# Optimization experiments

Hardware: AMD Instinct MI355X
Metric: run time of the kernel (lower is better)

## Reference

```python
import jax, jax.numpy as jnp
import numpy as np

EPS_LN = 1e-5
EPS_D = 1e-8
K = 3

def layer_norm(x, g, b):
    mu = jnp.mean(x, axis=-1, keepdims=True)
    var = jnp.var(x, axis=-1, keepdims=True)
    return (x - mu) * jax.lax.rsqrt(var + EPS_LN) * g + b

def setup_inputs() -> dict:
    key = jax.random.key(0)
    ks = jax.random.split(key, 8)
    Nc, Nu, Cin, Cout = 4096, 16384, 256, 256
    return {
        "x_feat": jax.random.normal(ks[0], (Nc, Cin), jnp.float32),
        "x_pos": jax.random.uniform(ks[1], (Nc, 3), jnp.float32),
        "xup_feat": jax.random.normal(ks[2], (Nu, Cout), jnp.float32),
        "xup_pos": jax.random.uniform(ks[3], (Nu, 3), jnp.float32),
        "g1": jnp.ones((Cin,), jnp.float32),
        "b1": jnp.zeros((Cin,), jnp.float32),
        "W": jax.random.normal(ks[4], (Cin, Cout), jnp.float32) * 0.02,
        "b": jnp.zeros((Cout,), jnp.float32),
        "g2": jnp.ones((Cout,), jnp.float32),
        "b2": jnp.zeros((Cout,), jnp.float32),
        "W_up": jax.random.normal(ks[5], (Cout, Cout), jnp.float32) * 0.02,
        "b_up": jnp.zeros((Cout,), jnp.float32),
    }

def reference(x_feat, x_pos, xup_feat, xup_pos, g1, b1, W, b, g2, b2, W_up, b_up):
    # norm -> linear on coarse points: [Nc, Cout]
    x = layer_norm(x_feat, g1, b1) @ W + b
    # norm -> linear on fine points:   [Nu, Cout]
    xu = layer_norm(xup_feat, g2, b2) @ W_up + b_up
    # squared pairwise distances fine->coarse: [Nu, Nc]
    d2 = (jnp.sum(xup_pos * xup_pos, axis=-1, keepdims=True)
          - 2.0 * (xup_pos @ x_pos.T)
          + jnp.sum(x_pos * x_pos, axis=-1))
    # k nearest coarse neighbors per fine point
    neg_d2, idx = jax.lax.top_k(-d2, K)          # [Nu, K]
    w = 1.0 / (-neg_d2 + EPS_D)                  # inverse-distance weights
    w = w / jnp.sum(w, axis=-1, keepdims=True)
    # gather + weighted sum: [Nu, Cout]
    interp = jnp.einsum('uk,ukc->uc', w, x[idx])
    return interp + xu
```

## Files before the change

kernel.cpp:

```cpp
#include <hip/hip_runtime.h>

#define EPS_LN 1e-5f
#define EPS_D  1e-8f
#define BIGD 3.402823466e+38f

typedef __attribute__((ext_vector_type(8))) short s16x8;
typedef __attribute__((ext_vector_type(4))) float f32x4;
typedef __attribute__((ext_vector_type(4))) unsigned short u16x4;

#define XC_OFF    0u
#define XH_OFF    4194304u
#define XL_OFF    14680064u
#define MU_OFF    25165824u
#define RS_OFF    25247744u
#define WGH_OFF   25329664u
#define WGL_OFF   25460736u
#define WUGH_OFF  25591808u
#define WUGL_OFF  25722880u
#define C12_OFF   25853952u
#define CPS_OFF   25858048u
#define IDXS_OFF  25923584u
#define CST_OFF   25939968u
#define UPS_OFF   25944064u
#define USORT_OFF 26206208u

__device__ __forceinline__ int cell_of(float px, float py, float pz) {
    int cx = (int)(px * 8.0f); cx = cx < 0 ? 0 : (cx > 7 ? 7 : cx);
    int cy = (int)(py * 8.0f); cy = cy < 0 ? 0 : (cy > 7 ? 7 : cy);
    int cz = (int)(pz * 8.0f); cz = cz < 0 ? 0 : (cz > 7 ? 7 : cz);
    return (cz * 8 + cy) * 8 + cx;
}

__global__ __launch_bounds__(256) void prep_kernel(
    const float* __restrict__ x_feat, const float* __restrict__ xup_feat,
    const float* __restrict__ x_pos, const float* __restrict__ xup_pos,
    const float* __restrict__ W, const float* __restrict__ W_up,
    const float* __restrict__ g1, const float* __restrict__ b1,
    const float* __restrict__ g2, const float* __restrict__ b2,
    float* __restrict__ mu, float* __restrict__ rs,
    unsigned short* __restrict__ xh, unsigned short* __restrict__ xl,
    unsigned short* __restrict__ wgh, unsigned short* __restrict__ wgl,
    unsigned short* __restrict__ wugh, unsigned short* __restrict__ wugl,
    float* __restrict__ c12,
    float4* __restrict__ cps, int* __restrict__ idxs, int* __restrict__ cellStart,
    float4* __restrict__ ups, int* __restrict__ usort)
{
    __shared__ int cnt[512];
    __shared__ int ofs[512];
    __shared__ int wpart[4];

    const int bid = blockIdx.x, tid = threadIdx.x;
    const int lane = tid & 63, wave = tid >> 6;

    if (bid < 640) {
        #pragma unroll
        for (int rr = 0; rr < 8; ++rr) {
            const int r = bid * 32 + wave * 8 + rr;
            const float* src = (r < 16384) ? (xup_feat + (size_t)r * 256)
                                           : (x_feat + (size_t)(r - 16384) * 256);
            const float4 v = ((const float4*)src)[lane];
            float s  = v.x + v.y + v.z + v.w;
            float ss = v.x*v.x + v.y*v.y + v.z*v.z + v.w*v.w;
            #pragma unroll
            for (int off = 1; off < 64; off <<= 1) {
                s  += __shfl_xor(s,  off);
                ss += __shfl_xor(ss, off);
            }
            if (lane == 0) {
                const float m   = s * (1.0f / 256.0f);
                const float var = ss * (1.0f / 256.0f) - m * m;
                mu[r] = m;
                rs[r] = rsqrtf(var + EPS_LN);
            }
            const float vv[4] = { v.x, v.y, v.z, v.w };
            u16x4 hv, lv;
            #pragma unroll
            for (int c = 0; c < 4; ++c) {
                const unsigned ua = __float_as_uint(vv[c]);
                hv[c] = (unsigned short)(ua >> 16);
                const float lo = vv[c] - __uint_as_float(ua & 0xFFFF0000u);
                lv[c] = (unsigned short)(__float_as_uint(lo) >> 16);
            }
            *(u16x4*)&xh[(size_t)r * 256 + lane * 4] = hv;
            *(u16x4*)&xl[(size_t)r * 256 + lane * 4] = lv;
        }
    } else if (bid < 656) {
        const int mb = bid - 640;
        const float* src = (mb < 8) ? W : W_up;
        const float* g   = (mb < 8) ? g1 : g2;
        unsigned short* dh = (mb < 8) ? wgh : wugh;
        unsigned short* dl = (mb < 8) ? wgl : wugl;
        const int n  = (mb & 7) * 32 + (tid >> 3);
        const int kc = (tid & 7) * 32;
        for (int kk = 0; kk < 32; kk += 4) {
            u16x4 hv, lv;
            #pragma unroll
            for (int c = 0; c < 4; ++c) {
                const int k = kc + kk + c;
                const float wv = g[k] * src[(size_t)k * 256 + n];
                const unsigned ua = __float_as_uint(wv);
                hv[c] = (unsigned short)(ua >> 16);
                const float lo = wv - __uint_as_float(ua & 0xFFFF0000u);
                lv[c] = (unsigned short)(__float_as_uint(lo) >> 16);
            }
            *(u16x4*)&dh[(size_t)n * 256 + kc + kk] = hv;
            *(u16x4*)&dl[(size_t)n * 256 + kc + kk] = lv;
        }
    } else if (bid < 658) {
        const bool fine = (bid == 657);
        const float* src = fine ? W_up : W;
        const float* g   = fine ? g2 : g1;
        const float* bln = fine ? b2 : b1;
        float* c1 = c12 + (fine ? 0 : 512);
        float* c2 = c12 + (fine ? 256 : 768);
        float a1 = 0.0f, a2 = 0.0f;
        for (int k = 0; k < 256; ++k) {
            const float wv = src[(size_t)k * 256 + tid];
            a1 = fmaf(bln[k], wv, a1);
            a2 = fmaf(g[k],   wv, a2);
        }
        c1[tid] = a1;
        c2[tid] = a2;
    } else {
        const bool fine = (bid == 659);
        const int npts = fine ? 16384 : 4096;
        const float* pos = fine ? xup_pos : x_pos;

        cnt[tid] = 0; cnt[tid + 256] = 0;
        __syncthreads();
        for (int i = tid; i < npts; i += 256) {
            const int c = cell_of(pos[i*3+0], pos[i*3+1], pos[i*3+2]);
            atomicAdd(&cnt[c], 1);
        }
        __syncthreads();
        const int base = wave * 128 + lane * 2;
        const int a = cnt[base], b = cnt[base + 1];
        const int p = a + b;
        int incl = p;
        #pragma unroll
        for (int off = 1; off < 64; off <<= 1) {
            const int t = __shfl_up(incl, off);
            if (lane >= off) incl += t;
        }
        if (lane == 63) wpart[wave] = incl;
        __syncthreads();
        int woff = 0;
        for (int w = 0; w < 4; ++w) if (w < wave) woff += wpart[w];
        const int e0 = woff + (incl - p);
        ofs[base] = e0;          ofs[base + 1] = e0 + a;
        if (!fine) {
            cellStart[base] = e0;    cellStart[base + 1] = e0 + a;
            if (tid == 0) cellStart[512] = 4096;
        }
        __syncthreads();
        for (int i = tid; i < npts; i += 256) {
            const float px = pos[i*3+0], py = pos[i*3+1], pz = pos[i*3+2];
            const int c = cell_of(px, py, pz);
            const int slot = atomicAdd(&ofs[c], 1);
            if (fine) {
                ups[slot] = make_float4(px, py, pz, px*px + py*py + pz*pz);
                usort[slot] = i;
            } else {
                cps[slot] = make_float4(px, py, pz, px*px + py*py + pz*pz);
                idxs[slot] = i;
            }
        }
    }
}

__global__ __launch_bounds__(256) void gemm_kernel(
    const unsigned short* __restrict__ xh, const unsigned short* __restrict__ xl,
    const float* __restrict__ mu, const float* __restrict__ rs,
    const unsigned short* __restrict__ wgh, const unsigned short* __restrict__ wgl,
    const unsigned short* __restrict__ wugh, const unsigned short* __restrict__ wugl,
    const float* __restrict__ c12,
    const float* __restrict__ b_up, const float* __restrict__ bb,
    float* __restrict__ outF, float* __restrict__ outC)
{
    const int bid = blockIdx.x;
    const unsigned short *BH, *BL; const float *c1, *c2, *bias; float* OUT;
    int row0, col0, statbase;
    if (bid < 256) {
        BH = wugh; BL = wugl; c1 = c12; c2 = c12 + 256; bias = b_up; OUT = outF;
        row0 = (bid >> 1) * 128; col0 = (bid & 1) * 128; statbase = 0;
    } else {
        const int id = bid - 256;
        BH = wgh; BL = wgl; c1 = c12 + 512; c2 = c12 + 768; bias = bb; OUT = outC;
        row0 = (id >> 1) * 128; col0 = (id & 1) * 128; statbase = 16384;
    }

    const int lane = threadIdx.x & 63;
    const int wave = threadIdx.x >> 6;
    const int wr = wave >> 1, wc = wave & 1;
    const int lm = lane & 15, lk = lane >> 4;

    int arow[4];
    #pragma unroll
    for (int mf = 0; mf < 4; ++mf)
        arow[mf] = statbase + row0 + wr * 64 + mf * 16 + lm;

    int ncol[4]; float c1v[4], c2v[4], bv[4];
    #pragma unroll
    for (int nf = 0; nf < 4; ++nf) {
        ncol[nf] = col0 + wc * 64 + nf * 16 + lm;
        c1v[nf] = c1[ncol[nf]];
        c2v[nf] = c2[ncol[nf]];
        bv[nf]  = bias[ncol[nf]];
    }

    f32x4 acc[4][4];
    #pragma unroll
    for (int mf = 0; mf < 4; ++mf)
        #pragma unroll
        for (int nf = 0; nf < 4; ++nf)
            acc[mf][nf] = (f32x4){0.0f, 0.0f, 0.0f, 0.0f};

    for (int k0 = 0; k0 < 256; k0 += 32) {
        const int kb = k0 + lk * 8;

        s16x8 bh[4], bl[4], ah[4], al[4];
        #pragma unroll
        for (int nf = 0; nf < 4; ++nf) {
            const size_t o = (size_t)ncol[nf] * 256 + kb;
            bh[nf] = *(const s16x8*)(BH + o);
            bl[nf] = *(const s16x8*)(BL + o);
        }
        #pragma unroll
        for (int mf = 0; mf < 4; ++mf) {
            const size_t o = (size_t)arow[mf] * 256 + kb;
            ah[mf] = *(const s16x8*)(xh + o);
            al[mf] = *(const s16x8*)(xl + o);
        }

        #pragma unroll
        for (int mf = 0; mf < 4; ++mf)
            #pragma unroll
            for (int nf = 0; nf < 4; ++nf) {
                acc[mf][nf] = __builtin_amdgcn_mfma_f32_16x16x32_bf16(ah[mf], bh[nf], acc[mf][nf], 0, 0, 0);
                acc[mf][nf] = __builtin_amdgcn_mfma_f32_16x16x32_bf16(ah[mf], bl[nf], acc[mf][nf], 0, 0, 0);
                acc[mf][nf] = __builtin_amdgcn_mfma_f32_16x16x32_bf16(al[mf], bh[nf], acc[mf][nf], 0, 0, 0);
            }
    }

    #pragma unroll
    for (int mf = 0; mf < 4; ++mf) {
        #pragma unroll
        for (int q = 0; q < 4; ++q) {
            const int orow = row0 + wr * 64 + mf * 16 + lk * 4 + q;
            const float m = mu[statbase + orow];
            const float s = rs[statbase + orow];
            const float ms = -m * s;
            #pragma unroll
            for (int nf = 0; nf < 4; ++nf)
                OUT[(size_t)orow * 256 + ncol[nf]] =
                    fmaf(s, acc[mf][nf][q], fmaf(ms, c2v[nf], c1v[nf]) + bv[nf]);
        }
    }
}

__device__ __forceinline__ void ins3(float d, int p,
    float& b0, float& b1, float& b2, int& p0, int& p1, int& p2)
{
    const bool lt0 = d < b0, lt1 = d < b1, lt2 = d < b2;
    const float n1 = lt0 ? b0 : (lt1 ? d : b1);
    const int   q1 = lt0 ? p0 : (lt1 ? p : p1);
    const float n2 = lt1 ? b1 : (lt2 ? d : b2);
    const int   q2 = lt1 ? p1 : (lt2 ? p : p2);
    b0 = lt0 ? d : b0;  p0 = lt0 ? p : p0;
    b1 = n1; p1 = q1;
    b2 = n2; p2 = q2;
}

__global__ __launch_bounds__(256) void topk_kernel(
    const float4* __restrict__ cps, const int* __restrict__ idxs,
    const int* __restrict__ cellStart,
    const float4* __restrict__ ups, const int* __restrict__ usort,
    const float* __restrict__ xc, float* __restrict__ out)
{
    __shared__ float pd[4][64][3];
    __shared__ int   pp[4][64][3];
    __shared__ float wsel[64][3];
    __shared__ int   isel[64][3];
    __shared__ int   uor[64];
    __shared__ int   cst[513];

    const int tid = threadIdx.x, lane = tid & 63, wave = tid >> 6;
    const int su = blockIdx.x * 64 + lane;

    for (int i = tid; i < 513; i += 256) cst[i] = cellStart[i];

    const float4 up = ups[su];
    const float ux = up.x, uy = up.y, uz = up.z, uu = up.w;
    if (wave == 0) uor[lane] = usort[su];
    int cx = (int)(ux * 8.0f); cx = cx < 0 ? 0 : (cx > 7 ? 7 : cx);
    int cy = (int)(uy * 8.0f); cy = cy < 0 ? 0 : (cy > 7 ? 7 : cy);
    int cz = (int)(uz * 8.0f); cz = cz < 0 ? 0 : (cz > 7 ? 7 : cz);

    __syncthreads();

    float b0 = BIGD, b1 = BIGD, b2 = BIGD;
    int p0 = 0, p1 = 0, p2 = 0;

    for (int cc = wave; cc < 27; cc += 4) {
        const int nx = cx + (cc % 3) - 1;
        const int ny = cy + ((cc / 3) % 3) - 1;
        const int nz = cz + (cc / 9) - 1;
        if ((unsigned)nx > 7u || (unsigned)ny > 7u || (unsigned)nz > 7u) continue;
        const int cell = (nz * 8 + ny) * 8 + nx;
        const int s = cst[cell], e = cst[cell + 1];
        if (s >= e) continue;
        float4 c = cps[s];
        for (int p = s; p < e; ++p) {
            const float4 nxt = (p + 1 < e) ? cps[p + 1] : c;
            const float dot = ux * c.x + uy * c.y + uz * c.z;
            const float d = (uu - 2.0f * dot) + c.w;
            ins3(d, p, b0, b1, b2, p0, p1, p2);
            c = nxt;
        }
    }

    pd[wave][lane][0] = b0; pd[wave][lane][1] = b1; pd[wave][lane][2] = b2;
    pp[wave][lane][0] = p0; pp[wave][lane][1] = p1; pp[wave][lane][2] = p2;
    __syncthreads();

    if (wave == 0) {
        for (int w = 1; w < 4; ++w) {
            #pragma unroll
            for (int e = 0; e < 3; ++e)
                ins3(pd[w][lane][e], pp[w][lane][e], b0, b1, b2, p0, p1, p2);
        }

        const float h = 0.125f;
        float gmin = BIGD;
        if (cx > 0) gmin = fminf(gmin, ux - (float)(cx - 1) * h);
        if (cx < 7) gmin = fminf(gmin, (float)(cx + 2) * h - ux);
        if (cy > 0) gmin = fminf(gmin, uy - (float)(cy - 1) * h);
        if (cy < 7) gmin = fminf(gmin, (float)(cy + 2) * h - uy);
        if (cz > 0) gmin = fminf(gmin, uz - (float)(cz - 1) * h);
        if (cz < 7) gmin = fminf(gmin, (float)(cz + 2) * h - uz);

        if (b2 > gmin * gmin) {
            b0 = b1 = b2 = BIGD; p0 = p1 = p2 = 0;
            for (int p = 0; p < 4096; ++p) {
                const float4 c = cps[p];
                const float dot = ux * c.x + uy * c.y + uz * c.z;
                const float d = (uu - 2.0f * dot) + c.w;
                ins3(d, p, b0, b1, b2, p0, p1, p2);
            }
        }

        float w0 = 1.0f / (b0 + EPS_D);
        float w1 = 1.0f / (b1 + EPS_D);
        float w2 = 1.0f / (b2 + EPS_D);
        const float inv = 1.0f / (w0 + w1 + w2);
        wsel[lane][0] = w0 * inv; wsel[lane][1] = w1 * inv; wsel[lane][2] = w2 * inv;
        isel[lane][0] = idxs[p0]; isel[lane][1] = idxs[p1]; isel[lane][2] = idxs[p2];
    }
    __syncthreads();

    #pragma unroll
    for (int r = 0; r < 16; ++r) {
        const int ul = wave * 16 + r;
        const float w0 = wsel[ul][0], w1 = wsel[ul][1], w2 = wsel[ul][2];
        const int a0 = isel[ul][0], a1 = isel[ul][1], a2 = isel[ul][2];
        const float4 v0 = ((const float4*)(xc + (size_t)a0 * 256))[lane];
        const float4 v1 = ((const float4*)(xc + (size_t)a1 * 256))[lane];
        const float4 v2 = ((const float4*)(xc + (size_t)a2 * 256))[lane];
        float4* op = (float4*)(out + (size_t)uor[ul] * 256);
        float4 o = op[lane];
        o.x += w0 * v0.x + w1 * v1.x + w2 * v2.x;
        o.y += w0 * v0.y + w1 * v1.y + w2 * v2.y;
        o.z += w0 * v0.z + w1 * v1.z + w2 * v2.z;
        o.w += w0 * v0.w + w1 * v1.w + w2 * v2.w;
        op[lane] = o;
    }
}

extern "C" void kernel_launch(void* const* d_in, const int* in_sizes, int n_in,
                              void* d_out, int out_size, void* d_ws, size_t ws_size,
                              hipStream_t stream)
{
    const float* x_feat   = (const float*)d_in[0];
    const float* x_pos    = (const float*)d_in[1];
    const float* xup_feat = (const float*)d_in[2];
    const float* xup_pos  = (const float*)d_in[3];
    const float* g1       = (const float*)d_in[4];
    const float* b1       = (const float*)d_in[5];
    const float* W        = (const float*)d_in[6];
    const float* bb       = (const float*)d_in[7];
    const float* g2       = (const float*)d_in[8];
    const float* b2       = (const float*)d_in[9];
    const float* W_up     = (const float*)d_in[10];
    const float* b_up     = (const float*)d_in[11];

    float* out = (float*)d_out;
    char*  ws  = (char*)d_ws;

    float* xc  = (float*)(ws + XC_OFF);
    unsigned short* xh   = (unsigned short*)(ws + XH_OFF);
    unsigned short* xl   = (unsigned short*)(ws + XL_OFF);
    float* mu  = (float*)(ws + MU_OFF);
    float* rs  = (float*)(ws + RS_OFF);
    unsigned short* wgh  = (unsigned short*)(ws + WGH_OFF);
    unsigned short* wgl  = (unsigned short*)(ws + WGL_OFF);
    unsigned short* wugh = (unsigned short*)(ws + WUGH_OFF);
    unsigned short* wugl = (unsigned short*)(ws + WUGL_OFF);
    float* c12 = (float*)(ws + C12_OFF);
    float4* cps = (float4*)(ws + CPS_OFF);
    int* idxs   = (int*)(ws + IDXS_OFF);
    int* cstart = (int*)(ws + CST_OFF);
    float4* ups = (float4*)(ws + UPS_OFF);
    int* usort  = (int*)(ws + USORT_OFF);

    prep_kernel<<<660, 256, 0, stream>>>(x_feat, xup_feat, x_pos, xup_pos,
                                         W, W_up, g1, b1, g2, b2,
                                         mu, rs, xh, xl,
                                         wgh, wgl, wugh, wugl,
                                         c12, cps, idxs, cstart, ups, usort);
    gemm_kernel<<<320, 256, 0, stream>>>(xh, xl, mu, rs,
                                         wgh, wgl, wugh, wugl,
                                         c12, b_up, bb, out, xc);
    topk_kernel<<<256, 256, 0, stream>>>(cps, idxs, cstart, ups, usort, xc, out);
}
```

Measured before the change: 192.4 us.

## Use 1024-thread prep blocks and schedule serial binning blocks first

The prep kernel now runs 168 blocks of 1024 threads instead of 660 blocks of 256. The long serial tasks (spatial binning of points and the c1/c2 bias reductions) move to the lowest block indices so they start first. The c1/c2 reduction is split four ways over k and summed in shared memory, and the scan covers 512 cells with 8 waves. This is meant to shorten the critical path of the binning and reduction blocks that previously trailed the row-wise layer-norm split work. In exchange, fewer and larger blocks may limit how many blocks fit per CU.

```diff
diff --git a/kernel.cpp b/kernel.cpp
--- a/kernel.cpp
+++ b/kernel.cpp
@@ -31,7 +31,7 @@
     return (cz * 8 + cy) * 8 + cx;
 }
 
-__global__ __launch_bounds__(256) void prep_kernel(
+__global__ __launch_bounds__(1024) void prep_kernel(
     const float* __restrict__ x_feat, const float* __restrict__ xup_feat,
     const float* __restrict__ x_pos, const float* __restrict__ xup_pos,
     const float* __restrict__ W, const float* __restrict__ W_up,
@@ -45,115 +45,55 @@
     float4* __restrict__ cps, int* __restrict__ idxs, int* __restrict__ cellStart,
     float4* __restrict__ ups, int* __restrict__ usort)
 {
-    __shared__ int cnt[512];
-    __shared__ int ofs[512];
-    __shared__ int wpart[4];
+    __shared__ float smemf[2048];
+    int* const cnt   = (int*)smemf;
+    int* const ofs   = ((int*)smemf) + 512;
+    __shared__ int wpart[8];
+    __shared__ int wpref[8];
 
     const int bid = blockIdx.x, tid = threadIdx.x;
     const int lane = tid & 63, wave = tid >> 6;
 
-    if (bid < 640) {
-        #pragma unroll
-        for (int rr = 0; rr < 8; ++rr) {
-            const int r = bid * 32 + wave * 8 + rr;
-            const float* src = (r < 16384) ? (xup_feat + (size_t)r * 256)
-                                           : (x_feat + (size_t)(r - 16384) * 256);
-            const float4 v = ((const float4*)src)[lane];
-            float s  = v.x + v.y + v.z + v.w;
-            float ss = v.x*v.x + v.y*v.y + v.z*v.z + v.w*v.w;
-            #pragma unroll
-            for (int off = 1; off < 64; off <<= 1) {
-                s  += __shfl_xor(s,  off);
-                ss += __shfl_xor(ss, off);
-            }
-            if (lane == 0) {
-                const float m   = s * (1.0f / 256.0f);
-                const float var = ss * (1.0f / 256.0f) - m * m;
-                mu[r] = m;
-                rs[r] = rsqrtf(var + EPS_LN);
-            }
-            const float vv[4] = { v.x, v.y, v.z, v.w };
-            u16x4 hv, lv;
-            #pragma unroll
-            for (int c = 0; c < 4; ++c) {
-                const unsigned ua = __float_as_uint(vv[c]);
-                hv[c] = (unsigned short)(ua >> 16);
-                const float lo = vv[c] - __uint_as_float(ua & 0xFFFF0000u);
-                lv[c] = (unsigned short)(__float_as_uint(lo) >> 16);
-            }
-            *(u16x4*)&xh[(size_t)r * 256 + lane * 4] = hv;
-            *(u16x4*)&xl[(size_t)r * 256 + lane * 4] = lv;
-        }
-    } else if (bid < 656) {
-        const int mb = bid - 640;
-        const float* src = (mb < 8) ? W : W_up;
-        const float* g   = (mb < 8) ? g1 : g2;
-        unsigned short* dh = (mb < 8) ? wgh : wugh;
-        unsigned short* dl = (mb < 8) ? wgl : wugl;
-        const int n  = (mb & 7) * 32 + (tid >> 3);
-        const int kc = (tid & 7) * 32;
-        for (int kk = 0; kk < 32; kk += 4) {
-            u16x4 hv, lv;
-            #pragma unroll
-            for (int c = 0; c < 4; ++c) {
-                const int k = kc + kk + c;
-                const float wv = g[k] * src[(size_t)k * 256 + n];
-                const unsigned ua = __float_as_uint(wv);
-                hv[c] = (unsigned short)(ua >> 16);
-                const float lo = wv - __uint_as_float(ua & 0xFFFF0000u);
-                lv[c] = (unsigned short)(__float_as_uint(lo) >> 16);
-            }
-            *(u16x4*)&dh[(size_t)n * 256 + kc + kk] = hv;
-            *(u16x4*)&dl[(size_t)n * 256 + kc + kk] = lv;
-        }
-    } else if (bid < 658) {
-        const bool fine = (bid == 657);
-        const float* src = fine ? W_up : W;
-        const float* g   = fine ? g2 : g1;
-        const float* bln = fine ? b2 : b1;
-        float* c1 = c12 + (fine ? 0 : 512);
-        float* c2 = c12 + (fine ? 256 : 768);
-        float a1 = 0.0f, a2 = 0.0f;
-        for (int k = 0; k < 256; ++k) {
-            const float wv = src[(size_t)k * 256 + tid];
-            a1 = fmaf(bln[k], wv, a1);
-            a2 = fmaf(g[k],   wv, a2);
-        }
-        c1[tid] = a1;
-        c2[tid] = a2;
-    } else {
-        const bool fine = (bid == 659);
+    if (bid < 2) {
+        const bool fine = (bid == 0);
         const int npts = fine ? 16384 : 4096;
         const float* pos = fine ? xup_pos : x_pos;
 
-        cnt[tid] = 0; cnt[tid + 256] = 0;
-        __syncthreads();
-        for (int i = tid; i < npts; i += 256) {
+        if (tid < 512) cnt[tid] = 0;
+        __syncthreads();
+        for (int i = tid; i < npts; i += 1024) {
             const int c = cell_of(pos[i*3+0], pos[i*3+1], pos[i*3+2]);
             atomicAdd(&cnt[c], 1);
         }
         __syncthreads();
-        const int base = wave * 128 + lane * 2;
-        const int a = cnt[base], b = cnt[base + 1];
-        const int p = a + b;
-        int incl = p;
-        #pragma unroll
-        for (int off = 1; off < 64; off <<= 1) {
-            const int t = __shfl_up(incl, off);
-            if (lane >= off) incl += t;
-        }
-        if (lane == 63) wpart[wave] = incl;
-        __syncthreads();
-        int woff = 0;
-        for (int w = 0; w < 4; ++w) if (w < wave) woff += wpart[w];
-        const int e0 = woff + (incl - p);
-        ofs[base] = e0;          ofs[base + 1] = e0 + a;
-        if (!fine) {
-            cellStart[base] = e0;    cellStart[base + 1] = e0 + a;
-            if (tid == 0) cellStart[512] = 4096;
-        }
-        __syncthreads();
-        for (int i = tid; i < npts; i += 256) {
+        int v = 0, incl = 0;
+        if (wave < 8) {
+            const int cell = wave * 64 + lane;
+            v = cnt[cell];
+            incl = v;
+            #pragma unroll
+            for (int off = 1; off < 64; off <<= 1) {
+                const int t = __shfl_up(incl, off);
+                if (lane >= off) incl += t;
+            }
+            if (lane == 63) wpart[wave] = incl;
+        }
+        __syncthreads();
+        if (tid == 0) {
+            int run = 0;
+            #pragma unroll
+            for (int w = 0; w < 8; ++w) { wpref[w] = run; run += wpart[w]; }
+        }
+        __syncthreads();
+        if (wave < 8) {
+            const int cell = wave * 64 + lane;
+            const int excl = incl - v + wpref[wave];
+            ofs[cell] = excl;
+            if (!fine) cellStart[cell] = excl;
+        }
+        if (!fine && tid == 0) cellStart[512] = 4096;
+        __syncthreads();
+        for (int i = tid; i < npts; i += 1024) {
             const float px = pos[i*3+0], py = pos[i*3+1], pz = pos[i*3+2];
             const int c = cell_of(px, py, pz);
             const int slot = atomicAdd(&ofs[c], 1);
@@ -164,6 +104,83 @@
                 cps[slot] = make_float4(px, py, pz, px*px + py*py + pz*pz);
                 idxs[slot] = i;
             }
+        }
+    } else if (bid < 4) {
+        const bool fine = (bid == 2);
+        const float* src = fine ? W_up : W;
+        const float* g   = fine ? g2 : g1;
+        const float* bln = fine ? b2 : b1;
+        float* c1 = c12 + (fine ? 0 : 512);
+        float* c2 = c12 + (fine ? 256 : 768);
+        const int col = tid & 255, kg = tid >> 8;
+        float a1 = 0.0f, a2 = 0.0f;
+        for (int k = kg * 64; k < kg * 64 + 64; ++k) {
+            const float wv = src[(size_t)k * 256 + col];
+            a1 = fmaf(bln[k], wv, a1);
+            a2 = fmaf(g[k],   wv, a2);
+        }
+        smemf[kg * 256 + col] = a1;
+        smemf[1024 + kg * 256 + col] = a2;
+        __syncthreads();
+        if (kg == 0) {
+            c1[col] = smemf[col] + smemf[256 + col] + smemf[512 + col] + smemf[768 + col];
+            c2[col] = smemf[1024 + col] + smemf[1280 + col] + smemf[1536 + col] + smemf[1792 + col];
+        }
+    } else if (bid < 8) {
+        const int mb = (bid - 4) * 4 + (tid >> 8);
+        const int t = tid & 255;
+        const float* src = (mb < 8) ? W : W_up;
+        const float* g   = (mb < 8) ? g1 : g2;
+        unsigned short* dh = (mb < 8) ? wgh : wugh;
+        unsigned short* dl = (mb < 8) ? wgl : wugl;
+        const int n  = (mb & 7) * 32 + (t >> 3);
+        const int kc = (t & 7) * 32;
+        for (int kk = 0; kk < 32; kk += 4) {
+            u16x4 hv, lv;
+            #pragma unroll
+            for (int c = 0; c < 4; ++c) {
+                const int k = kc + kk + c;
+                const float wv = g[k] * src[(size_t)k * 256 + n];
+                const unsigned ua = __float_as_uint(wv);
+                hv[c] = (unsigned short)(ua >> 16);
+                const float lo = wv - __uint_as_float(ua & 0xFFFF0000u);
+                lv[c] = (unsigned short)(__float_as_uint(lo) >> 16);
+            }
+            *(u16x4*)&dh[(size_t)n * 256 + kc + kk] = hv;
+            *(u16x4*)&dl[(size_t)n * 256 + kc + kk] = lv;
+        }
+    } else {
+        const int rbase = (bid - 8) * 128 + wave * 8;
+        #pragma unroll
+        for (int rr = 0; rr < 8; ++rr) {
+            const int r = rbase + rr;
+            const float* src = (r < 16384) ? (xup_feat + (size_t)r * 256)
+                                           : (x_feat + (size_t)(r - 16384) * 256);
+            const float4 v = ((const float4*)src)[lane];
+            float s  = v.x + v.y + v.z + v.w;
+            float ss = v.x*v.x + v.y*v.y + v.z*v.z + v.w*v.w;
+            #pragma unroll
+            for (int off = 1; off < 64; off <<= 1) {
+                s  += __shfl_xor(s,  off);
+                ss += __shfl_xor(ss, off);
+            }
+            if (lane == 0) {
+                const float m   = s * (1.0f / 256.0f);
+                const float var = ss * (1.0f / 256.0f) - m * m;
+                mu[r] = m;
+                rs[r] = rsqrtf(var + EPS_LN);
+            }
+            const float vv[4] = { v.x, v.y, v.z, v.w };
+            u16x4 hv, lv;
+            #pragma unroll
+            for (int c = 0; c < 4; ++c) {
+                const unsigned ua = __float_as_uint(vv[c]);
+                hv[c] = (unsigned short)(ua >> 16);
+                const float lo = vv[c] - __uint_as_float(ua & 0xFFFF0000u);
+                lv[c] = (unsigned short)(__float_as_uint(lo) >> 16);
+            }
+            *(u16x4*)&xh[(size_t)r * 256 + lane * 4] = hv;
+            *(u16x4*)&xl[(size_t)r * 256 + lane * 4] = lv;
         }
     }
 }
@@ -412,11 +429,11 @@
     float4* ups = (float4*)(ws + UPS_OFF);
     int* usort  = (int*)(ws + USORT_OFF);
 
-    prep_kernel<<<660, 256, 0, stream>>>(x_feat, xup_feat, x_pos, xup_pos,
-                                         W, W_up, g1, b1, g2, b2,
-                                         mu, rs, xh, xl,
-                                         wgh, wgl, wugh, wugl,
-                                         c12, cps, idxs, cstart, ups, usort);
+    prep_kernel<<<168, 1024, 0, stream>>>(x_feat, xup_feat, x_pos, xup_pos,
+                                          W, W_up, g1, b1, g2, b2,
+                                          mu, rs, xh, xl,
+                                          wgh, wgl, wugh, wugl,
+                                          c12, cps, idxs, cstart, ups, usort);
     gemm_kernel<<<320, 256, 0, stream>>>(xh, xl, mu, rs,
                                          wgh, wgl, wugh, wugl,
                                          c12, b_up, bb, out, xc);
```

Result: faster. 180.5 us (-6.2%).
